# Kernel tuning notes

Hardware: AMD Instinct MI355X
Metric: run time of the kernel (lower is better)

## Reference

```python
import jax, jax.numpy as jnp
import numpy as np

N, T, B = 307, 12, 32
H, E, K, HEADS = 64, 10, 2, 4
HD = H // HEADS
HORIZON = 12


def _layer_norm(x, g, b, eps=1e-5):
    m = jnp.mean(x, -1, keepdims=True)
    v = jnp.var(x, -1, keepdims=True)
    return (x - m) * jax.lax.rsqrt(v + eps) * g + b


def _pos_emb(t_len, d):
    pos = np.arange(t_len)[:, None].astype(np.float32)
    i = np.arange(0, d, 2)[None, :].astype(np.float32)
    ang = pos / np.power(10000.0, i / d)
    pe = np.zeros((t_len, d), np.float32)
    pe[:, 0::2] = np.sin(ang)
    pe[:, 1::2] = np.cos(ang)
    return jnp.asarray(pe)


def setup_inputs() -> dict:
    key = jax.random.key(0)
    ks = iter(jax.random.split(key, 40))

    def rn(shape, scale=0.1):
        return jax.random.normal(next(ks), shape, jnp.float32) * scale

    return {
        'source': rn((B, T, N, 1), 1.0),
        'node_emb': rn((N, E), 1.0),
        'gate_w0': rn((E, K, 1 + H, 2 * H)), 'gate_b0': rn((E, 2 * H)),
        'upd_w0': rn((E, K, 1 + H, H)), 'upd_b0': rn((E, H)),
        'gate_w1': rn((E, K, 2 * H, 2 * H)), 'gate_b1': rn((E, 2 * H)),
        'upd_w1': rn((E, K, 2 * H, H)), 'upd_b1': rn((E, H)),
        'mlp_w': rn((1, H)), 'mlp_b': rn((H,)),
        'wq': rn((H, H)), 'bq': rn((H,)),
        'wk': rn((H, H)), 'bk': rn((H,)),
        'wv': rn((H, H)), 'bv': rn((H,)),
        'wo': rn((H, H)), 'bo': rn((H,)),
        'ffn_w1': rn((H, 1024)), 'ffn_b1': rn((1024,)),
        'ffn_w2': rn((1024, H)), 'ffn_b2': rn((H,)),
        'ln1_g': jnp.ones((H,), jnp.float32), 'ln1_b': jnp.zeros((H,), jnp.float32),
        'ln2_g': jnp.ones((H,), jnp.float32), 'ln2_b': jnp.zeros((H,), jnp.float32),
        'ws': rn((N, H)), 'wt': rn((N, H)),
        'conv_w': rn((HORIZON, H)), 'conv_b': rn((HORIZON,)),
    }


def reference(source, node_emb, gate_w0, gate_b0, upd_w0, upd_b0,
              gate_w1, gate_b1, upd_w1, upd_b1, mlp_w, mlp_b,
              wq, bq, wk, bk, wv, bv, wo, bo,
              ffn_w1, ffn_b1, ffn_w2, ffn_b2,
              ln1_g, ln1_b, ln2_g, ln2_b, ws, wt, conv_w, conv_b):
    dt = source.dtype
    # adaptive supports: [I, softmax(relu(E E^T))]  (cheb_k = 2)
    A = jax.nn.softmax(jax.nn.relu(node_emb @ node_emb.T), axis=1)
    supports = jnp.stack([jnp.eye(N, dtype=dt), A.astype(dt)])  # (K,N,N)

    def run_layer(xs, wg, bg, wu, bu):
        # per-node weights from embedding pools (computed once per layer)
        Wg = jnp.einsum('ne,ekio->nkio', node_emb, wg)
        Bg = node_emb @ bg
        Wu = jnp.einsum('ne,ekio->nkio', node_emb, wu)
        Bu = node_emb @ bu

        def gconv(inp, Wn, Bn):
            xg = jnp.einsum('knm,bmc->bnkc', supports, inp)
            return jnp.einsum('bnki,nkio->bno', xg, Wn) + Bn

        def step(h, x_t):
            zr = jax.nn.sigmoid(gconv(jnp.concatenate([x_t, h], -1), Wg, Bg))
            z, r = jnp.split(zr, 2, axis=-1)
            hc = jnp.tanh(gconv(jnp.concatenate([x_t, z * h], -1), Wu, Bu))
            h_new = r * h + (1.0 - r) * hc
            return h_new, h_new

        h0 = jnp.zeros((xs.shape[0], N, H), dt)
        _, hs = jax.lax.scan(step, h0, jnp.swapaxes(xs, 0, 1))
        return jnp.swapaxes(hs, 0, 1)  # (B,T,N,H)

    out = run_layer(source, gate_w0, gate_b0, upd_w0, upd_b0)
    out = run_layer(out, gate_w1, gate_b1, upd_w1, upd_b1)
    output_1 = out[:, -1:]  # (B,1,N,H)

    # temporal self-attention branch
    x = source @ mlp_w + mlp_b + _pos_emb(T, H)[None, :, None, :]  # (B,T,N,H)
    xb = x.transpose(0, 2, 1, 3).reshape(B * N, T, H)
    q = (xb @ wq + bq).reshape(-1, T, HEADS, HD)
    k = (xb @ wk + bk).reshape(-1, T, HEADS, HD)
    v = (xb @ wv + bv).reshape(-1, T, HEADS, HD)
    scores = jnp.einsum('bthd,bshd->bhts', q, k) / jnp.sqrt(jnp.asarray(HD, dt))
    attn = jax.nn.softmax(scores, axis=-1)
    o = jnp.einsum('bhts,bshd->bthd', attn, v).reshape(-1, T, H)
    o = _layer_norm(xb + (o @ wo + bo), ln1_g, ln1_b)
    f = jax.nn.relu(o @ ffn_w1 + ffn_b1) @ ffn_w2 + ffn_b2
    o = _layer_norm(o + f, ln2_g, ln2_b)
    output_2 = o.reshape(B, N, T, H).transpose(0, 2, 1, 3)[:, -1:]  # (B,1,N,H)

    comb = output_1 * ws + output_2 * wt  # (B,1,N,H)
    # end_conv: Conv2d(1, horizon, kernel=(1,H)) == linear over H
    y = jnp.einsum('bnh,oh->bon', comb[:, 0], conv_w) + conv_b[None, :, None]  # (B,12,N)
    return y.reshape(B, HORIZON, 1, N).transpose(0, 1, 3, 2)  # (B,12,N,1)
```

## Files before the change

kernel.cpp:

```cpp
#include <hip/hip_runtime.h>
#include <hip/hip_bf16.h>

typedef __hip_bfloat16 bf16;

constexpr int NN = 307, TT = 12, BB = 32, HH = 64, EE = 10, HEADS = 4, HD = 16, HORIZON = 12;

constexpr int S_SRC = 0,       S_EMB = 117888,  S_GW0 = 120958,  S_GB0 = 287358,
              S_UW0 = 288638,  S_UB0 = 371838,  S_GW1 = 372478,  S_GB1 = 700158,
              S_UW1 = 701438,  S_UB1 = 865278,  S_MLW = 865918,  S_MLB = 865982,
              S_WQ  = 866046,  S_BQ  = 870142,  S_WK  = 870206,  S_BK  = 874302,
              S_WV  = 874366,  S_BV  = 878462,  S_WO  = 878526,  S_BO  = 882622,
              S_FW1 = 882686,  S_FB1 = 948222,  S_FW2 = 949246,  S_FB2 = 1014782,
              S_L1G = 1014846, S_L1B = 1014910, S_L2G = 1014974, S_L2B = 1015038,
              S_WS  = 1015102, S_WT  = 1034750, S_CW  = 1054398, S_CB  = 1055166;

constexpr size_t OFF_A    = 1055178;
constexpr size_t OFF_OUT0 = 1149427;
constexpr size_t OFF_H0   = 8694259;
constexpr size_t OFF_ZH0  = 9322995;
constexpr size_t OFF_R0   = 9951731;
constexpr size_t OFF_AX0  = 11209203;
constexpr size_t OFF_AX1  = 11327091;
constexpr size_t OFF_PE   = 18871923;
constexpr size_t OFF_OLN  = 18872691;
constexpr size_t OFF_O2   = 19501427;
constexpr size_t OFF_WB   = 20130164;

constexpr size_t G0X = OFF_WB +        0;
constexpr size_t G0H = OFF_WB +    78592;
constexpr size_t BG0 = OFF_WB +  5108480;
constexpr size_t U0X = OFF_WB +  5147776;
constexpr size_t U0H = OFF_WB +  5187072;
constexpr size_t BU0 = OFF_WB +  7702016;
constexpr size_t G1X = OFF_WB +  7721664;
constexpr size_t G1H = OFF_WB + 12751552;
constexpr size_t BG1 = OFF_WB + 17781440;
constexpr size_t U1X = OFF_WB + 17820736;
constexpr size_t U1H = OFF_WB + 20335680;
constexpr size_t BU1 = OFF_WB + 22850624;
constexpr size_t OFF_GXP = OFF_WB + 22870272;
constexpr size_t OFF_UXP = OFF_GXP + 15089664;
constexpr size_t OFF_H1  = OFF_UXP + 7544832;
constexpr size_t OFF_ZH1 = OFF_H1  + 628736;
constexpr size_t OFF_R1  = OFF_ZH1 + 628736;
constexpr size_t OFF_AGG0 = OFF_R1  + 628736;
constexpr size_t OFF_AGG1 = OFF_AGG0 + 628736;
constexpr size_t OFF_AT   = OFF_AGG1 + 628736;
constexpr size_t G_TOTAL  = OFF_AT + 94249 + 4096;


__device__ float g_buf[G_TOTAL];
__device__ int g_flag;

__device__ __forceinline__ float wave_sum(float v) {
    #pragma unroll
    for (int off = 32; off > 0; off >>= 1) v += __shfl_xor(v, off, 64);
    return v;
}

__global__ void k_detect(const void* emb_raw) {
    const bf16* p = (const bf16*)emb_raw;
    int lane = threadIdx.x;
    float v = __bfloat162float(p[lane]);
    bool plaus = (v == v) && (fabsf(v) <= 1e4f) && (v == 0.f || fabsf(v) >= 1e-4f);
    float c = wave_sum(plaus ? 1.f : 0.f);
    if (lane == 0) g_flag = (c >= 52.f) ? 1 : 0;
}

struct PtrPack { const void* p[32]; };
__device__ const int D_CNT[32] = {117888,3070,166400,1280,83200,640,327680,1280,163840,640,
                                  64,64,4096,64,4096,64,4096,64,4096,64,
                                  65536,1024,65536,64,64,64,64,64,19648,19648,768,12};
__device__ const int D_OFF[32] = {S_SRC,S_EMB,S_GW0,S_GB0,S_UW0,S_UB0,S_GW1,S_GB1,S_UW1,S_UB1,
                                  S_MLW,S_MLB,S_WQ,S_BQ,S_WK,S_BK,S_WV,S_BV,S_WO,S_BO,
                                  S_FW1,S_FB1,S_FW2,S_FB2,S_L1G,S_L1B,S_L2G,S_L2B,S_WS,S_WT,S_CW,S_CB};
__device__ const int D_CHK[33] = {0,461,473,1123,1128,1453,1456,2736,2741,3381,3384,3385,3386,
                                  3402,3403,3419,3420,3436,3437,3453,3454,3710,3714,3970,3971,
                                  3972,3973,3974,3975,4052,4129,4132,4133};

__global__ void k_ingest(PtrPack pk) {
    int bid = blockIdx.x;
    int s = 0;
    while (s < 31 && bid >= D_CHK[s + 1]) s++;
    int i = (bid - D_CHK[s]) * 256 + threadIdx.x;
    if (i >= D_CNT[s]) return;
    float v;
    if (g_flag) v = __bfloat162float(((const bf16*)pk.p[s])[i]);
    else        v = ((const float*)pk.p[s])[i];
    g_buf[(size_t)D_OFF[s] + i] = v;
}

__global__ void k_adj() {
    int n = blockIdx.x;
    int tid = threadIdx.x;
    __shared__ float en[EE];
    __shared__ float red[512];
    if (tid < EE) en[tid] = g_buf[S_EMB + n * EE + tid];
    __syncthreads();
    bool act = tid < NN;
    float d = 0.f;
    if (act) {
        #pragma unroll
        for (int e = 0; e < EE; e++) d += en[e] * g_buf[S_EMB + tid * EE + e];
        d = fmaxf(d, 0.f);
    }
    red[tid] = act ? d : -1e30f;
    __syncthreads();
    for (int s = 256; s > 0; s >>= 1) { if (tid < s) red[tid] = fmaxf(red[tid], red[tid + s]); __syncthreads(); }
    float mx = red[0];
    __syncthreads();
    float ex = act ? expf(d - mx) : 0.f;
    red[tid] = ex;
    __syncthreads();
    for (int s = 256; s > 0; s >>= 1) { if (tid < s) red[tid] += red[tid + s]; __syncthreads(); }
    float inv = 1.f / red[0];
    if (act) {
        float av = ex * inv;
        g_buf[OFF_A  + (size_t)n * NN + tid] = av;
        g_buf[OFF_AT + (size_t)tid * NN + n] = av;
    }
}

__global__ void k_nodew_all() {
    unsigned i4 = blockIdx.x * 256u + threadIdx.x;
    if (i4 >= 5717568u) return;
    float a0 = 0.f, a1 = 0.f, a2 = 0.f, a3 = 0.f;
    size_t dst;
    unsigned n;

    #define NW_ACCUM(SRCOFF, JCONST) do {                                  \
        const float* eb = g_buf + S_EMB + n * EE;                          \
        const float* wp = g_buf + (SRCOFF) + j;                            \
        _Pragma("unroll")                                                  \
        for (int e = 0; e < EE; e++) {                                     \
            float ev = eb[e];                                              \
            a0 += ev * wp[0]; a1 += ev * wp[1];                            \
            a2 += ev * wp[2]; a3 += ev * wp[3];                            \
            wp += (JCONST);                                                \
        }                                                                  \
    } while (0)

    if (i4 < 1277120u) {
        unsigned rem = i4;
        n = rem / 4160u;
        unsigned j = (rem - n * 4160u) * 4u;
        unsigned o = j & 127u, kk = j >> 7;
        unsigned k = (kk >= 65u) ? 1u : 0u, i = kk - k * 65u;
        dst = (i == 0u) ? G0X + ((size_t)(n * 2u + k)) * 128u + o
                        : G0H + ((size_t)(n * 128u + k * 64u + (i - 1u))) * 128u + o;
        NW_ACCUM(S_GW0, 16640u);
    } else if (i4 < 1286944u) {
        unsigned rem = i4 - 1277120u;
        n = rem >> 5;
        unsigned j = (rem & 31u) * 4u;
        dst = BG0 + (size_t)n * 128u + j;
        NW_ACCUM(S_GB0, 128u);
    } else if (i4 < 1925504u) {
        unsigned rem = i4 - 1286944u;
        n = rem / 2080u;
        unsigned j = (rem - n * 2080u) * 4u;
        unsigned o = j & 63u, kk = j >> 6;
        unsigned k = (kk >= 65u) ? 1u : 0u, i = kk - k * 65u;
        dst = (i == 0u) ? U0X + ((size_t)(n * 2u + k)) * 64u + o
                        : U0H + ((size_t)(n * 128u + k * 64u + (i - 1u))) * 64u + o;
        NW_ACCUM(S_UW0, 8320u);
    } else if (i4 < 1930416u) {
        unsigned rem = i4 - 1925504u;
        n = rem >> 4;
        unsigned j = (rem & 15u) * 4u;
        dst = BU0 + (size_t)n * 64u + j;
        NW_ACCUM(S_UB0, 64u);
    } else if (i4 < 4445360u) {
        unsigned rem = i4 - 1930416u;
        n = rem >> 13;
        unsigned j = (rem & 8191u) * 4u;
        unsigned o = j & 127u, kk = j >> 7;
        unsigned k = kk >> 7, i = kk & 127u;
        dst = (i < 64u) ? G1X + ((size_t)(n * 128u + k * 64u + i)) * 128u + o
                        : G1H + ((size_t)(n * 128u + k * 64u + (i - 64u))) * 128u + o;
        NW_ACCUM(S_GW1, 32768u);
    } else if (i4 < 4455184u) {
        unsigned rem = i4 - 4445360u;
        n = rem >> 5;
        unsigned j = (rem & 31u) * 4u;
        dst = BG1 + (size_t)n * 128u + j;
        NW_ACCUM(S_GB1, 128u);
    } else if (i4 < 5712656u) {
        unsigned rem = i4 - 4455184u;
        n = rem >> 12;
        unsigned j = (rem & 4095u) * 4u;
        unsigned o = j & 63u, kk = j >> 6;
        unsigned k = kk >> 7, i = kk & 127u;
        dst = (i < 64u) ? U1X + ((size_t)(n * 128u + k * 64u + i)) * 64u + o
                        : U1H + ((size_t)(n * 128u + k * 64u + (i - 64u))) * 64u + o;
        NW_ACCUM(S_UW1, 16384u);
    } else {
        unsigned rem = i4 - 5712656u;
        n = rem >> 4;
        unsigned j = (rem & 15u) * 4u;
        dst = BU1 + (size_t)n * 64u + j;
        NW_ACCUM(S_UB1, 64u);
    }
    #undef NW_ACCUM
    *(float4*)&g_buf[dst] = make_float4(a0, a1, a2, a3);
}

__global__ void k_pe() {
    int tid = threadIdx.x;
    int t = tid >> 6, h = tid & 63;
    float ex = (float)(h & ~1) / 64.f;
    float ang = (float)t * powf(10000.f, -ex);
    g_buf[OFF_PE + tid] = (h & 1) ? cosf(ang) : sinf(ang);
}

__global__ void k_zero(size_t off, int cnt) {
    int i = blockIdx.x * 256 + threadIdx.x;
    if (i < cnt) g_buf[off + i] = 0.f;
}

__global__ __launch_bounds__(256) void k_ax0() {
    int t = blockIdx.y;
    int n0 = blockIdx.x * 8;
    int b = threadIdx.x & 31, nl = threadIdx.x >> 5;
    __shared__ float As[8][68];
    __shared__ float xs[32][65];
    float acc = 0.f;
    for (int m0 = 0; m0 < NN; m0 += 64) {
        int jend = min(64, NN - m0);
        for (int idx = threadIdx.x; idx < 8 * 64; idx += 256) {
            int i = idx >> 6, jj = idx & 63;
            int n = n0 + i, m = m0 + jj;
            As[i][jj] = (n < NN && m < NN) ? g_buf[OFF_A + (size_t)n * NN + m] : 0.f;
        }
        for (int idx = threadIdx.x; idx < 32 * 64; idx += 256) {
            int bb = idx >> 6, jj = idx & 63;
            int m = m0 + jj;
            xs[bb][jj] = (m < NN) ? g_buf[S_SRC + ((size_t)bb * TT + t) * NN + m] : 0.f;
        }
        __syncthreads();
        for (int jj = 0; jj < jend; jj++) acc += As[nl][jj] * xs[b][jj];
        __syncthreads();
    }
    int n = n0 + nl;
    if (n < NN) g_buf[OFF_AX0 + ((size_t)t * NN + n) * 32 + b] = acc;
}

__global__ __launch_bounds__(256) void k_aggB(int s, int mode) {
    int z = blockIdx.z;
    size_t srcOff, dstOff;
    float* __restrict__ dstp2 = nullptr;
    if (mode == 0) {
        if (z == 0) { srcOff = OFF_H0; dstOff = OFF_AGG0;
                      dstp2 = g_buf + OFF_AX1 + (size_t)(s - 1) * 628736; }
        else        { srcOff = OFF_H1; dstOff = OFF_AGG1; }
    } else {
        srcOff = z ? OFF_ZH1 : OFF_ZH0;
        dstOff = z ? OFF_AGG1 : OFF_AGG0;
    }
    const float* __restrict__ srcp = g_buf + srcOff;
    float* __restrict__ dstp = g_buf + dstOff;
    int n0 = blockIdx.x * 64;
    int col0 = blockIdx.y * 64;
    int tid = threadIdx.x;
    int tn = tid >> 4, tc = tid & 15;
    __shared__ float As[64][68];
    __shared__ float Xs[64][64];
    float acc[4][4];
    #pragma unroll
    for (int i = 0; i < 4; i++)
        #pragma unroll
        for (int j = 0; j < 4; j++) acc[i][j] = 0.f;
    for (int k0 = 0; k0 < NN; k0 += 64) {
        for (int idx = tid; idx < 64 * 64; idx += 256) {
            int i = idx & 63, k = idx >> 6;
            int n = n0 + i, m = k0 + k;
            As[k][i] = (n < NN && m < NN) ? g_buf[OFF_AT + (size_t)m * NN + n] : 0.f;
        }
        for (int idx = tid; idx < 64 * 16; idx += 256) {
            int c4 = idx & 15, k = idx >> 4;
            int m = k0 + k;
            float4 v = (m < NN) ? *(const float4*)&srcp[(size_t)m * 2048 + col0 + c4 * 4]
                                : make_float4(0.f, 0.f, 0.f, 0.f);
            *(float4*)&Xs[k][c4 * 4] = v;
        }
        __syncthreads();
        #pragma unroll
        for (int k = 0; k < 64; k++) {
            float4 a4 = *(const float4*)&As[k][tn * 4];
            float4 x4 = *(const float4*)&Xs[k][tc * 4];
            const float* aa = (const float*)&a4;
            const float* xx = (const float*)&x4;
            #pragma unroll
            for (int i = 0; i < 4; i++)
                #pragma unroll
                for (int j = 0; j < 4; j++) acc[i][j] += aa[i] * xx[j];
        }
        __syncthreads();
    }
    #pragma unroll
    for (int i = 0; i < 4; i++) {
        int n = n0 + tn * 4 + i;
        if (n < NN) {
            float4 v = make_float4(acc[i][0], acc[i][1], acc[i][2], acc[i][3]);
            size_t doff = (size_t)n * 2048 + col0 + tc * 4;
            *(float4*)&dstp[doff] = v;
            if (dstp2) *(float4*)&dstp2[doff] = v;
        }
    }
}

__global__ __launch_bounds__(256) void k_xprep0() {
    int t = blockIdx.x, n = blockIdx.y, tid = threadIdx.x;
    __shared__ float xv[32], ax[32];
    if (tid < 32) {
        xv[tid] = g_buf[S_SRC + ((size_t)tid * TT + t) * NN + n];
        ax[tid] = g_buf[OFF_AX0 + ((size_t)t * NN + n) * 32 + tid];
    }
    __syncthreads();
    size_t pbase = ((size_t)t * NN + n) * 32;
    for (int idx = tid; idx < 4096; idx += 256) {
        int b = idx >> 7, o = idx & 127;
        g_buf[OFF_GXP + (pbase + b) * 128 + o] =
            g_buf[BG0 + (size_t)n * 128 + o]
          + g_buf[G0X + ((size_t)n * 2 + 0) * 128 + o] * xv[b]
          + g_buf[G0X + ((size_t)n * 2 + 1) * 128 + o] * ax[b];
    }
    for (int idx = tid; idx < 2048; idx += 256) {
        int b = idx >> 6, o = idx & 63;
        g_buf[OFF_UXP + (pbase + b) * 64 + o] =
            g_buf[BU0 + (size_t)n * 64 + o]
          + g_buf[U0X + ((size_t)n * 2 + 0) * 64 + o] * xv[b]
          + g_buf[U0X + ((size_t)n * 2 + 1) * 64 + o] * ax[b];
    }
}

__global__ __launch_bounds__(256) void k_gateM(int s) {
    __shared__ float smem[8704];
    float* xh = smem;
    float* xx = smem + 4352;
    int lay = (blockIdx.x >= NN) ? 1 : 0;
    int n = blockIdx.x - lay * NN;
    int t = lay ? (s - 1) : s;
    if (t < 0 || t >= TT) return;
    int tid = threadIdx.x;
    size_t Hoff = lay ? OFF_H1 : OFF_H0;
    size_t Aoff = lay ? OFF_AGG1 : OFF_AGG0;
    for (int idx = tid; idx < 4096; idx += 256) {
        int bl = idx >> 7, c = idx & 127;
        float v = (c < 64) ? g_buf[Hoff + (size_t)n * 2048 + bl * 64 + c]
                           : g_buf[Aoff + (size_t)n * 2048 + bl * 64 + (c - 64)];
        xh[bl * 136 + c] = v;
    }
    if (lay) {
        size_t pb = ((size_t)t * NN + n) * 2048;
        for (int idx = tid; idx < 4096; idx += 256) {
            int bl = idx >> 7, c = idx & 127;
            float v = (c < 64) ? g_buf[OFF_OUT0 + pb + bl * 64 + c]
                               : g_buf[OFF_AX1 + pb + bl * 64 + (c - 64)];
            xx[bl * 136 + c] = v;
        }
    }
    __syncthreads();
    int o = tid & 63, bl0 = (tid >> 6) * 8;
    size_t pbase = ((size_t)t * NN + n) * 32;
    float accz[8], accr[8];
    if (lay) {
        #pragma unroll
        for (int j = 0; j < 8; j++) {
            accz[j] = g_buf[BG1 + (size_t)n * 128 + o];
            accr[j] = g_buf[BG1 + (size_t)n * 128 + o + 64];
        }
    } else {
        #pragma unroll
        for (int j = 0; j < 8; j++) {
            accz[j] = g_buf[OFF_GXP + (pbase + bl0 + j) * 128 + o];
            accr[j] = g_buf[OFF_GXP + (pbase + bl0 + j) * 128 + o + 64];
        }
    }

#define GATE_MAC(WP, XP)                                                       \
    _Pragma("unroll 2")                                                        \
    for (int kq = 0; kq < 128; kq += 4) {                                      \
        float w00 = (WP)[(kq + 0) * 128 + o], w01 = (WP)[(kq + 0) * 128 + o + 64]; \
        float w10 = (WP)[(kq + 1) * 128 + o], w11 = (WP)[(kq + 1) * 128 + o + 64]; \
        float w20 = (WP)[(kq + 2) * 128 + o], w21 = (WP)[(kq + 2) * 128 + o + 64]; \
        float w30 = (WP)[(kq + 3) * 128 + o], w31 = (WP)[(kq + 3) * 128 + o + 64]; \
        _Pragma("unroll")                                                      \
        for (int j = 0; j < 8; j++) {                                          \
            float4 xv = *(const float4*)&(XP)[(bl0 + j) * 136 + kq];           \
            accz[j] += xv.x * w00 + xv.y * w10 + xv.z * w20 + xv.w * w30;      \
            accr[j] += xv.x * w01 + xv.y * w11 + xv.z * w21 + xv.w * w31;      \
        }                                                                      \
    }

    if (lay) {
        const float* __restrict__ W0 = g_buf + G1X + (size_t)n * 16384;
        GATE_MAC(W0, xx);
        if (t > 0) {
            const float* __restrict__ W1 = g_buf + G1H + (size_t)n * 16384;
            GATE_MAC(W1, xh);
        }
    } else if (t > 0) {
        const float* __restrict__ W0 = g_buf + G0H + (size_t)n * 16384;
        GATE_MAC(W0, xh);
    }
#undef GATE_MAC

    size_t ZHoff = lay ? OFF_ZH1 : OFF_ZH0;
    size_t Roff  = lay ? OFF_R1 : OFF_R0;
    #pragma unroll
    for (int j = 0; j < 8; j++) {
        int b = bl0 + j;
        float z = 1.f / (1.f + expf(-accz[j]));
        float r = 1.f / (1.f + expf(-accr[j]));
        float hv = xh[b * 136 + o];
        g_buf[ZHoff + (size_t)n * 2048 + (size_t)b * 64 + o] = z * hv;
        g_buf[Roff  + (size_t)n * 2048 + (size_t)b * 64 + o] = r;
    }
}

__global__ __launch_bounds__(256) void k_updM(int s) {
    __shared__ float smem[8704];
    float* xh = smem;
    float* xx = smem + 4352;
    int lay = (blockIdx.x >= NN) ? 1 : 0;
    int n = blockIdx.x - lay * NN;
    int t = lay ? (s - 1) : s;
    if (t < 0 || t >= TT) return;
    int tid = threadIdx.x;
    size_t ZHoff = lay ? OFF_ZH1 : OFF_ZH0;
    size_t Aoff  = lay ? OFF_AGG1 : OFF_AGG0;
    for (int idx = tid; idx < 4096; idx += 256) {
        int bl = idx >> 7, c = idx & 127;
        float v = (c < 64) ? g_buf[ZHoff + (size_t)n * 2048 + bl * 64 + c]
                           : g_buf[Aoff + (size_t)n * 2048 + bl * 64 + (c - 64)];
        xh[bl * 136 + c] = v;
    }
    if (lay) {
        size_t pb = ((size_t)t * NN + n) * 2048;
        for (int idx = tid; idx < 4096; idx += 256) {
            int bl = idx >> 7, c = idx & 127;
            float v = (c < 64) ? g_buf[OFF_OUT0 + pb + bl * 64 + c]
                               : g_buf[OFF_AX1 + pb + bl * 64 + (c - 64)];
            xx[bl * 136 + c] = v;
        }
    }
    __syncthreads();
    int o = tid & 63, bl0 = (tid >> 6) * 8;
    size_t pbase = ((size_t)t * NN + n) * 32;
    float acc[8];
    if (lay) {
        #pragma unroll
        for (int j = 0; j < 8; j++) acc[j] = g_buf[BU1 + (size_t)n * 64 + o];
    } else {
        #pragma unroll
        for (int j = 0; j < 8; j++) acc[j] = g_buf[OFF_UXP + (pbase + bl0 + j) * 64 + o];
    }

#define UPD_MAC(WP, XP)                                                        \
    _Pragma("unroll 2")                                                        \
    for (int kq = 0; kq < 128; kq += 4) {                                      \
        float w0 = (WP)[(kq + 0) * 64 + o];                                    \
        float w1 = (WP)[(kq + 1) * 64 + o];                                    \
        float w2 = (WP)[(kq + 2) * 64 + o];                                    \
        float w3 = (WP)[(kq + 3) * 64 + o];                                    \
        _Pragma("unroll")                                                      \
        for (int j = 0; j < 8; j++) {                                          \
            float4 xv = *(const float4*)&(XP)[(bl0 + j) * 136 + kq];           \
            acc[j] += xv.x * w0 + xv.y * w1 + xv.z * w2 + xv.w * w3;           \
        }                                                                      \
    }

    if (lay) {
        const float* __restrict__ W0 = g_buf + U1X + (size_t)n * 8192;
        UPD_MAC(W0, xx);
        if (t > 0) {
            const float* __restrict__ W1 = g_buf + U1H + (size_t)n * 8192;
            UPD_MAC(W1, xh);
        }
    } else if (t > 0) {
        const float* __restrict__ W0 = g_buf + U0H + (size_t)n * 8192;
        UPD_MAC(W0, xh);
    }
#undef UPD_MAC

    size_t Hoff = lay ? OFF_H1 : OFF_H0;
    size_t Roff = lay ? OFF_R1 : OFF_R0;
    #pragma unroll
    for (int j = 0; j < 8; j++) {
        int b = bl0 + j;
        size_t base = (size_t)n * 2048 + (size_t)b * 64 + o;
        float hc = tanhf(acc[j]);
        float r = g_buf[Roff + base];
        float hold = g_buf[Hoff + base];
        float hn = r * hold + (1.f - r) * hc;
        g_buf[Hoff + base] = hn;
        if (!lay) g_buf[OFF_OUT0 + (pbase + b) * 64 + o] = hn;
    }
}

__global__ __launch_bounds__(256) void k_attn() {
    int wid = threadIdx.x >> 6;
    int lane = threadIdx.x & 63;
    int g = blockIdx.x * 4 + wid;
    int b = g / NN, n = g - b * NN;
    __shared__ float x[4][TT][HH], kk[4][TT][HH], vv[4][TT][HH];
    __shared__ float q[4][HH], o1[4][HH], sc[4][HEADS][TT], aw[4][HEADS][TT];
    float mw = g_buf[S_MLW + lane];
    float mb = g_buf[S_MLB + lane];
    #pragma unroll
    for (int tt = 0; tt < TT; tt++) {
        float s = g_buf[S_SRC + ((size_t)b * TT + tt) * NN + n];
        x[wid][tt][lane] = s * mw + mb + g_buf[OFF_PE + tt * HH + lane];
    }
    __syncthreads();
    float ka[TT], va[TT];
    #pragma unroll
    for (int tt = 0; tt < TT; tt++) { ka[tt] = g_buf[S_BK + lane]; va[tt] = g_buf[S_BV + lane]; }
    float qa = g_buf[S_BQ + lane];
    for (int i0 = 0; i0 < HH; i0 += 4) {
        float wk0 = g_buf[S_WK + (i0 + 0) * HH + lane];
        float wk1 = g_buf[S_WK + (i0 + 1) * HH + lane];
        float wk2 = g_buf[S_WK + (i0 + 2) * HH + lane];
        float wk3 = g_buf[S_WK + (i0 + 3) * HH + lane];
        float wv0 = g_buf[S_WV + (i0 + 0) * HH + lane];
        float wv1 = g_buf[S_WV + (i0 + 1) * HH + lane];
        float wv2 = g_buf[S_WV + (i0 + 2) * HH + lane];
        float wv3 = g_buf[S_WV + (i0 + 3) * HH + lane];
        float wq0 = g_buf[S_WQ + (i0 + 0) * HH + lane];
        float wq1 = g_buf[S_WQ + (i0 + 1) * HH + lane];
        float wq2 = g_buf[S_WQ + (i0 + 2) * HH + lane];
        float wq3 = g_buf[S_WQ + (i0 + 3) * HH + lane];
        float4 xq = *(const float4*)&x[wid][TT - 1][i0];
        qa += xq.x * wq0 + xq.y * wq1 + xq.z * wq2 + xq.w * wq3;
        #pragma unroll
        for (int tt = 0; tt < TT; tt++) {
            float4 xv4 = *(const float4*)&x[wid][tt][i0];
            ka[tt] += xv4.x * wk0 + xv4.y * wk1 + xv4.z * wk2 + xv4.w * wk3;
            va[tt] += xv4.x * wv0 + xv4.y * wv1 + xv4.z * wv2 + xv4.w * wv3;
        }
    }
    #pragma unroll
    for (int tt = 0; tt < TT; tt++) { kk[wid][tt][lane] = ka[tt]; vv[wid][tt][lane] = va[tt]; }
    q[wid][lane] = qa;
    __syncthreads();
    if (lane < HEADS * TT) {
        int head = lane / TT, ts = lane - head * TT;
        float s = 0.f;
        #pragma unroll
        for (int d = 0; d < HD; d++) s += q[wid][head * HD + d] * kk[wid][ts][head * HD + d];
        sc[wid][head][ts] = s * 0.25f;
    }
    __syncthreads();
    if (lane < HEADS * TT) {
        int head = lane / TT, ts = lane - head * TT;
        float mx = -1e30f;
        #pragma unroll
        for (int j = 0; j < TT; j++) mx = fmaxf(mx, sc[wid][head][j]);
        float sm = 0.f;
        #pragma unroll
        for (int j = 0; j < TT; j++) sm += expf(sc[wid][head][j] - mx);
        aw[wid][head][ts] = expf(sc[wid][head][ts] - mx) / sm;
    }
    __syncthreads();
    int head = lane >> 4;
    float oa = 0.f;
    #pragma unroll
    for (int tt = 0; tt < TT; tt++) oa += aw[wid][head][tt] * vv[wid][tt][lane];
    o1[wid][lane] = oa;
    __syncthreads();
    float acc = g_buf[S_BO + lane];
    for (int i0 = 0; i0 < HH; i0 += 4) {
        float w0 = g_buf[S_WO + (i0 + 0) * HH + lane];
        float w1 = g_buf[S_WO + (i0 + 1) * HH + lane];
        float w2 = g_buf[S_WO + (i0 + 2) * HH + lane];
        float w3 = g_buf[S_WO + (i0 + 3) * HH + lane];
        float4 ov = *(const float4*)&o1[wid][i0];
        acc += ov.x * w0 + ov.y * w1 + ov.z * w2 + ov.w * w3;
    }
    float res = x[wid][TT - 1][lane] + acc;
    float mean = wave_sum(res) * (1.f / 64.f);
    float dv = res - mean;
    float var = wave_sum(dv * dv) * (1.f / 64.f);
    float ln = dv * rsqrtf(var + 1e-5f) * g_buf[S_L1G + lane] + g_buf[S_L1B + lane];
    g_buf[OFF_OLN + ((size_t)b * NN + n) * HH + lane] = ln;
}

__global__ __launch_bounds__(256) void k_ffn() {
    int tok0 = blockIdx.x * 8;
    int tid = threadIdx.x;
    int lane = tid & 63, wvid = tid >> 6;
    __shared__ float ox[8][HH];
    __shared__ float hid[8][1024];
    for (int idx = tid; idx < 8 * HH; idx += 256) {
        int tk = idx >> 6, hh = idx & 63;
        ox[tk][hh] = g_buf[OFF_OLN + (size_t)(tok0 + tk) * HH + hh];
    }
    __syncthreads();
    {
        float acc[4][8];
        #pragma unroll
        for (int p = 0; p < 4; p++) {
            float bj = g_buf[S_FB1 + tid + 256 * p];
            #pragma unroll
            for (int tk = 0; tk < 8; tk++) acc[p][tk] = bj;
        }
        for (int i0 = 0; i0 < HH; i0 += 4) {
            float w1r[4][4];
            #pragma unroll
            for (int qq = 0; qq < 4; qq++)
                #pragma unroll
                for (int p = 0; p < 4; p++)
                    w1r[p][qq] = g_buf[S_FW1 + (size_t)(i0 + qq) * 1024 + tid + 256 * p];
            #pragma unroll
            for (int tk = 0; tk < 8; tk++) {
                float4 xo = *(const float4*)&ox[tk][i0];
                const float* xp = (const float*)&xo;
                #pragma unroll
                for (int p = 0; p < 4; p++)
                    acc[p][tk] += xp[0] * w1r[p][0] + xp[1] * w1r[p][1]
                                + xp[2] * w1r[p][2] + xp[3] * w1r[p][3];
            }
        }
        #pragma unroll
        for (int p = 0; p < 4; p++)
            #pragma unroll
            for (int tk = 0; tk < 8; tk++)
                hid[tk][tid + 256 * p] = fmaxf(acc[p][tk], 0.f);
    }
    __syncthreads();
    float pa[8], pb[8];
    #pragma unroll
    for (int tk = 0; tk < 8; tk++) { pa[tk] = 0.f; pb[tk] = 0.f; }
    {
        int jbase = wvid * 256;
        #pragma unroll 2
        for (int j4 = 0; j4 < 256; j4 += 4) {
            int j0 = jbase + j4;
            float w0 = g_buf[S_FW2 + (size_t)(j0 + 0) * HH + lane];
            float w1 = g_buf[S_FW2 + (size_t)(j0 + 1) * HH + lane];
            float w2 = g_buf[S_FW2 + (size_t)(j0 + 2) * HH + lane];
            float w3 = g_buf[S_FW2 + (size_t)(j0 + 3) * HH + lane];
            #pragma unroll
            for (int tk = 0; tk < 8; tk++) {
                float4 h4 = *(const float4*)&hid[tk][j0];
                pa[tk] += h4.x * w0 + h4.y * w1;
                pb[tk] += h4.z * w2 + h4.w * w3;
            }
        }
    }
    __syncthreads();
    {
        float* rp = &hid[0][0];
        #pragma unroll
        for (int tk = 0; tk < 8; tk++)
            rp[(wvid * 8 + tk) * 64 + lane] = pa[tk] + pb[tk];
    }
    __syncthreads();
    int tk = wvid, hh = lane;
    float acc0 = g_buf[S_FB2 + hh], acc1 = acc0;
    {
        const float* rp = &hid[0][0];
        #pragma unroll
        for (int w = 0; w < 4; w++) {
            acc0 += rp[(w * 8 + tk) * 64 + hh];
            acc1 += rp[(w * 8 + tk + 4) * 64 + hh];
        }
    }
    #pragma unroll
    for (int ph = 0; ph < 2; ph++) {
        int tkk = tk + 4 * ph;
        float res = ox[tkk][hh] + (ph ? acc1 : acc0);
        float mean = wave_sum(res) * (1.f / 64.f);
        float dv = res - mean;
        float var = wave_sum(dv * dv) * (1.f / 64.f);
        float ln = dv * rsqrtf(var + 1e-5f) * g_buf[S_L2G + hh] + g_buf[S_L2B + hh];
        g_buf[OFF_O2 + (size_t)(tok0 + tkk) * HH + hh] = ln;
    }
}

__global__ void k_final(void* out) {
    int n = blockIdx.x, b = blockIdx.y;
    int h = threadIdx.x;
    __shared__ float comb[HH];
    comb[h] = g_buf[OFF_H1 + ((size_t)n * 32 + b) * 64 + h] * g_buf[S_WS + n * HH + h]
            + g_buf[OFF_O2 + ((size_t)b * NN + n) * 64 + h] * g_buf[S_WT + n * HH + h];
    __syncthreads();
    if (h < HORIZON) {
        float acc = g_buf[S_CB + h];
        #pragma unroll
        for (int i = 0; i < HH; i++) acc += comb[i] * g_buf[S_CW + h * HH + i];
        size_t oi = ((size_t)b * HORIZON + h) * NN + n;
        if (g_flag) ((bf16*)out)[oi] = __float2bfloat16(acc);
        else        ((float*)out)[oi] = acc;
    }
}

extern "C" void kernel_launch(void* const* d_in, const int* in_sizes, int n_in,
                              void* d_out, int out_size, void* d_ws, size_t ws_size,
                              hipStream_t stream) {
    PtrPack pk;
    for (int i = 0; i < 32; i++) pk.p[i] = d_in[i];

    k_detect<<<1, 64, 0, stream>>>(d_in[1]);
    k_ingest<<<4133, 256, 0, stream>>>(pk);
    k_adj<<<NN, 512, 0, stream>>>();
    k_nodew_all<<<22335, 256, 0, stream>>>();
    k_pe<<<1, 768, 0, stream>>>();
    k_ax0<<<dim3(39, 12), 256, 0, stream>>>();
    k_xprep0<<<dim3(12, NN), 256, 0, stream>>>();
    k_zero<<<2456, 256, 0, stream>>>(OFF_H0, 628736);
    k_zero<<<2456, 256, 0, stream>>>(OFF_H1, 628736);

    k_gateM<<<2 * NN, 256, 0, stream>>>(0);
    k_updM<<<2 * NN, 256, 0, stream>>>(0);
    for (int s = 1; s <= TT; s++) {
        k_aggB<<<dim3(5, 32, 2), 256, 0, stream>>>(s, 0);
        k_gateM<<<2 * NN, 256, 0, stream>>>(s);
        k_aggB<<<dim3(5, 32, 2), 256, 0, stream>>>(s, 1);
        k_updM<<<2 * NN, 256, 0, stream>>>(s);
    }

    k_attn<<<2456, 256, 0, stream>>>();
    k_ffn<<<1228, 256, 0, stream>>>();
    k_final<<<dim3(NN, BB), 64, 0, stream>>>(d_out);
}
```

Before: 2.155 ms.

## Split GRU recurrence kernels across more blocks and drop hidden-state zeroing

The per-step aggregation kernel now tiles 32 nodes per block instead of 64. The gate kernel is split over a second grid dimension into z and r halves, and the update kernel into two batch halves, which doubles the block count on the serial recurrence path for better occupancy. The zero-fill launches for hidden state are removed and replaced by treating the old state as zero at t==0. In exchange, the gate halves redundantly reload the same shared input tile, and each thread gets less register reuse.

```diff
diff --git a/kernel.cpp b/kernel.cpp
--- a/kernel.cpp
+++ b/kernel.cpp
@@ -213,11 +213,6 @@
     g_buf[OFF_PE + tid] = (h & 1) ? cosf(ang) : sinf(ang);
 }
 
-__global__ void k_zero(size_t off, int cnt) {
-    int i = blockIdx.x * 256 + threadIdx.x;
-    if (i < cnt) g_buf[off + i] = 0.f;
-}
-
 __global__ __launch_bounds__(256) void k_ax0() {
     int t = blockIdx.y;
     int n0 = blockIdx.x * 8;
@@ -259,20 +254,20 @@
     }
     const float* __restrict__ srcp = g_buf + srcOff;
     float* __restrict__ dstp = g_buf + dstOff;
-    int n0 = blockIdx.x * 64;
+    int n0 = blockIdx.x * 32;
     int col0 = blockIdx.y * 64;
     int tid = threadIdx.x;
     int tn = tid >> 4, tc = tid & 15;
-    __shared__ float As[64][68];
+    __shared__ float As[64][34];
     __shared__ float Xs[64][64];
-    float acc[4][4];
-    #pragma unroll
-    for (int i = 0; i < 4; i++)
+    float acc[2][4];
+    #pragma unroll
+    for (int i = 0; i < 2; i++)
         #pragma unroll
         for (int j = 0; j < 4; j++) acc[i][j] = 0.f;
     for (int k0 = 0; k0 < NN; k0 += 64) {
-        for (int idx = tid; idx < 64 * 64; idx += 256) {
-            int i = idx & 63, k = idx >> 6;
+        for (int idx = tid; idx < 64 * 32; idx += 256) {
+            int i = idx & 31, k = idx >> 5;
             int n = n0 + i, m = k0 + k;
             As[k][i] = (n < NN && m < NN) ? g_buf[OFF_AT + (size_t)m * NN + n] : 0.f;
         }
@@ -286,20 +281,21 @@
         __syncthreads();
         #pragma unroll
         for (int k = 0; k < 64; k++) {
-            float4 a4 = *(const float4*)&As[k][tn * 4];
+            float a0 = As[k][tn * 2];
+            float a1 = As[k][tn * 2 + 1];
             float4 x4 = *(const float4*)&Xs[k][tc * 4];
-            const float* aa = (const float*)&a4;
             const float* xx = (const float*)&x4;
             #pragma unroll
-            for (int i = 0; i < 4; i++)
-                #pragma unroll
-                for (int j = 0; j < 4; j++) acc[i][j] += aa[i] * xx[j];
+            for (int j = 0; j < 4; j++) {
+                acc[0][j] += a0 * xx[j];
+                acc[1][j] += a1 * xx[j];
+            }
         }
         __syncthreads();
     }
     #pragma unroll
-    for (int i = 0; i < 4; i++) {
-        int n = n0 + tn * 4 + i;
+    for (int i = 0; i < 2; i++) {
+        int n = n0 + tn * 2 + i;
         if (n < NN) {
             float4 v = make_float4(acc[i][0], acc[i][1], acc[i][2], acc[i][3]);
             size_t doff = (size_t)n * 2048 + col0 + tc * 4;
@@ -340,6 +336,7 @@
     float* xx = smem + 4352;
     int lay = (blockIdx.x >= NN) ? 1 : 0;
     int n = blockIdx.x - lay * NN;
+    int half = blockIdx.y;
     int t = lay ? (s - 1) : s;
     if (t < 0 || t >= TT) return;
     int tid = threadIdx.x;
@@ -362,34 +359,30 @@
     }
     __syncthreads();
     int o = tid & 63, bl0 = (tid >> 6) * 8;
+    int oc = half * 64 + o;
     size_t pbase = ((size_t)t * NN + n) * 32;
-    float accz[8], accr[8];
+    float acc[8];
     if (lay) {
-        #pragma unroll
-        for (int j = 0; j < 8; j++) {
-            accz[j] = g_buf[BG1 + (size_t)n * 128 + o];
-            accr[j] = g_buf[BG1 + (size_t)n * 128 + o + 64];
-        }
+        float b0 = g_buf[BG1 + (size_t)n * 128 + oc];
+        #pragma unroll
+        for (int j = 0; j < 8; j++) acc[j] = b0;
     } else {
         #pragma unroll
-        for (int j = 0; j < 8; j++) {
-            accz[j] = g_buf[OFF_GXP + (pbase + bl0 + j) * 128 + o];
-            accr[j] = g_buf[OFF_GXP + (pbase + bl0 + j) * 128 + o + 64];
-        }
+        for (int j = 0; j < 8; j++)
+            acc[j] = g_buf[OFF_GXP + (pbase + bl0 + j) * 128 + oc];
     }
 
 #define GATE_MAC(WP, XP)                                                       \
     _Pragma("unroll 2")                                                        \
     for (int kq = 0; kq < 128; kq += 4) {                                      \
-        float w00 = (WP)[(kq + 0) * 128 + o], w01 = (WP)[(kq + 0) * 128 + o + 64]; \
-        float w10 = (WP)[(kq + 1) * 128 + o], w11 = (WP)[(kq + 1) * 128 + o + 64]; \
-        float w20 = (WP)[(kq + 2) * 128 + o], w21 = (WP)[(kq + 2) * 128 + o + 64]; \
-        float w30 = (WP)[(kq + 3) * 128 + o], w31 = (WP)[(kq + 3) * 128 + o + 64]; \
+        float w0 = (WP)[(kq + 0) * 128 + oc];                                  \
+        float w1 = (WP)[(kq + 1) * 128 + oc];                                  \
+        float w2 = (WP)[(kq + 2) * 128 + oc];                                  \
+        float w3 = (WP)[(kq + 3) * 128 + oc];                                  \
         _Pragma("unroll")                                                      \
         for (int j = 0; j < 8; j++) {                                          \
             float4 xv = *(const float4*)&(XP)[(bl0 + j) * 136 + kq];           \
-            accz[j] += xv.x * w00 + xv.y * w10 + xv.z * w20 + xv.w * w30;      \
-            accr[j] += xv.x * w01 + xv.y * w11 + xv.z * w21 + xv.w * w31;      \
+            acc[j] += xv.x * w0 + xv.y * w1 + xv.z * w2 + xv.w * w3;           \
         }                                                                      \
     }
 
@@ -406,55 +399,67 @@
     }
 #undef GATE_MAC
 
-    size_t ZHoff = lay ? OFF_ZH1 : OFF_ZH0;
-    size_t Roff  = lay ? OFF_R1 : OFF_R0;
-    #pragma unroll
-    for (int j = 0; j < 8; j++) {
-        int b = bl0 + j;
-        float z = 1.f / (1.f + expf(-accz[j]));
-        float r = 1.f / (1.f + expf(-accr[j]));
-        float hv = xh[b * 136 + o];
-        g_buf[ZHoff + (size_t)n * 2048 + (size_t)b * 64 + o] = z * hv;
-        g_buf[Roff  + (size_t)n * 2048 + (size_t)b * 64 + o] = r;
+    if (half == 0) {
+        size_t ZHoff = lay ? OFF_ZH1 : OFF_ZH0;
+        #pragma unroll
+        for (int j = 0; j < 8; j++) {
+            int b = bl0 + j;
+            float zz = 1.f / (1.f + expf(-acc[j]));
+            float hv = (t == 0) ? 0.f : xh[b * 136 + o];
+            g_buf[ZHoff + (size_t)n * 2048 + (size_t)b * 64 + o] = zz * hv;
+        }
+    } else {
+        size_t Roff = lay ? OFF_R1 : OFF_R0;
+        #pragma unroll
+        for (int j = 0; j < 8; j++) {
+            int b = bl0 + j;
+            float r = 1.f / (1.f + expf(-acc[j]));
+            g_buf[Roff + (size_t)n * 2048 + (size_t)b * 64 + o] = r;
+        }
     }
 }
 
 __global__ __launch_bounds__(256) void k_updM(int s) {
-    __shared__ float smem[8704];
+    __shared__ float smem[4352];
     float* xh = smem;
-    float* xx = smem + 4352;
+    float* xx = smem + 2176;
     int lay = (blockIdx.x >= NN) ? 1 : 0;
     int n = blockIdx.x - lay * NN;
+    int half = blockIdx.y;
     int t = lay ? (s - 1) : s;
     if (t < 0 || t >= TT) return;
     int tid = threadIdx.x;
     size_t ZHoff = lay ? OFF_ZH1 : OFF_ZH0;
     size_t Aoff  = lay ? OFF_AGG1 : OFF_AGG0;
-    for (int idx = tid; idx < 4096; idx += 256) {
+    for (int idx = tid; idx < 2048; idx += 256) {
         int bl = idx >> 7, c = idx & 127;
-        float v = (c < 64) ? g_buf[ZHoff + (size_t)n * 2048 + bl * 64 + c]
-                           : g_buf[Aoff + (size_t)n * 2048 + bl * 64 + (c - 64)];
+        int bg = half * 16 + bl;
+        float v = (c < 64) ? g_buf[ZHoff + (size_t)n * 2048 + bg * 64 + c]
+                           : g_buf[Aoff + (size_t)n * 2048 + bg * 64 + (c - 64)];
         xh[bl * 136 + c] = v;
     }
     if (lay) {
         size_t pb = ((size_t)t * NN + n) * 2048;
-        for (int idx = tid; idx < 4096; idx += 256) {
+        for (int idx = tid; idx < 2048; idx += 256) {
             int bl = idx >> 7, c = idx & 127;
-            float v = (c < 64) ? g_buf[OFF_OUT0 + pb + bl * 64 + c]
-                               : g_buf[OFF_AX1 + pb + bl * 64 + (c - 64)];
+            int bg = half * 16 + bl;
+            float v = (c < 64) ? g_buf[OFF_OUT0 + pb + bg * 64 + c]
+                               : g_buf[OFF_AX1 + pb + bg * 64 + (c - 64)];
             xx[bl * 136 + c] = v;
         }
     }
     __syncthreads();
-    int o = tid & 63, bl0 = (tid >> 6) * 8;
+    int o = tid & 63, bl0 = (tid >> 6) * 4;
     size_t pbase = ((size_t)t * NN + n) * 32;
-    float acc[8];
+    float acc[4];
     if (lay) {
-        #pragma unroll
-        for (int j = 0; j < 8; j++) acc[j] = g_buf[BU1 + (size_t)n * 64 + o];
+        float b0 = g_buf[BU1 + (size_t)n * 64 + o];
+        #pragma unroll
+        for (int j = 0; j < 4; j++) acc[j] = b0;
     } else {
         #pragma unroll
-        for (int j = 0; j < 8; j++) acc[j] = g_buf[OFF_UXP + (pbase + bl0 + j) * 64 + o];
+        for (int j = 0; j < 4; j++)
+            acc[j] = g_buf[OFF_UXP + (pbase + half * 16 + bl0 + j) * 64 + o];
     }
 
 #define UPD_MAC(WP, XP)                                                        \
@@ -465,7 +470,7 @@
         float w2 = (WP)[(kq + 2) * 64 + o];                                    \
         float w3 = (WP)[(kq + 3) * 64 + o];                                    \
         _Pragma("unroll")                                                      \
-        for (int j = 0; j < 8; j++) {                                          \
+        for (int j = 0; j < 4; j++) {                                          \
             float4 xv = *(const float4*)&(XP)[(bl0 + j) * 136 + kq];           \
             acc[j] += xv.x * w0 + xv.y * w1 + xv.z * w2 + xv.w * w3;           \
         }                                                                      \
@@ -487,15 +492,15 @@
     size_t Hoff = lay ? OFF_H1 : OFF_H0;
     size_t Roff = lay ? OFF_R1 : OFF_R0;
     #pragma unroll
-    for (int j = 0; j < 8; j++) {
-        int b = bl0 + j;
-        size_t base = (size_t)n * 2048 + (size_t)b * 64 + o;
+    for (int j = 0; j < 4; j++) {
+        int bg = half * 16 + bl0 + j;
+        size_t base = (size_t)n * 2048 + (size_t)bg * 64 + o;
         float hc = tanhf(acc[j]);
         float r = g_buf[Roff + base];
-        float hold = g_buf[Hoff + base];
+        float hold = (t == 0) ? 0.f : g_buf[Hoff + base];
         float hn = r * hold + (1.f - r) * hc;
         g_buf[Hoff + base] = hn;
-        if (!lay) g_buf[OFF_OUT0 + (pbase + b) * 64 + o] = hn;
+        if (!lay) g_buf[OFF_OUT0 + (pbase + bg) * 64 + o] = hn;
     }
 }
 
@@ -709,16 +714,14 @@
     k_pe<<<1, 768, 0, stream>>>();
     k_ax0<<<dim3(39, 12), 256, 0, stream>>>();
     k_xprep0<<<dim3(12, NN), 256, 0, stream>>>();
-    k_zero<<<2456, 256, 0, stream>>>(OFF_H0, 628736);
-    k_zero<<<2456, 256, 0, stream>>>(OFF_H1, 628736);
-
-    k_gateM<<<2 * NN, 256, 0, stream>>>(0);
-    k_updM<<<2 * NN, 256, 0, stream>>>(0);
+
+    k_gateM<<<dim3(2 * NN, 2), 256, 0, stream>>>(0);
+    k_updM<<<dim3(2 * NN, 2), 256, 0, stream>>>(0);
     for (int s = 1; s <= TT; s++) {
-        k_aggB<<<dim3(5, 32, 2), 256, 0, stream>>>(s, 0);
-        k_gateM<<<2 * NN, 256, 0, stream>>>(s);
-        k_aggB<<<dim3(5, 32, 2), 256, 0, stream>>>(s, 1);
-        k_updM<<<2 * NN, 256, 0, stream>>>(s);
+        k_aggB<<<dim3(10, 32, 2), 256, 0, stream>>>(s, 0);
+        k_gateM<<<dim3(2 * NN, 2), 256, 0, stream>>>(s);
+        k_aggB<<<dim3(10, 32, 2), 256, 0, stream>>>(s, 1);
+        k_updM<<<dim3(2 * NN, 2), 256, 0, stream>>>(s);
     }
 
     k_attn<<<2456, 256, 0, stream>>>();
```

Measured after the change: 1.855 ms. 13.9% less time.
